# Kernel tuning notes

Measured on AMD Instinct MI355X. Metric: run time of the kernel, lower is better.

The kernel has to match this reference:

```python
import jax, jax.numpy as jnp
import numpy as np

DIM, A, B_FAC, BATCH = 256, 8, 8, 2048
IN_F, OUT_F = A * DIM, B_FAC * DIM  # 2048, 2048


def _make_masks():
    ri = np.arange(IN_F) // A       # input block index per row
    cj = np.arange(OUT_F) // B_FAC  # output block index per col
    diag = ri[:, None] == cj[None, :]
    off = ri[:, None] < cj[None, :]
    return diag, off

DIAG_NP, OFF_NP = _make_masks()
DIAG_M = jnp.asarray(DIAG_NP)
OFF_M = jnp.asarray(OFF_NP)


def setup_inputs() -> dict:
    key = jax.random.key(0)
    k1, k2, k3, k4 = jax.random.split(key, 4)
    x = jax.random.normal(k1, (BATCH, IN_F), dtype=jnp.float32)
    accum_blocks = jax.random.normal(k2, (BATCH, DIM, A, A), dtype=jnp.float32)
    # parameter init mirrors the torch module
    w = jax.random.normal(k3, (IN_F, OUT_F), dtype=jnp.float32) / np.sqrt(IN_F + OUT_F)
    weight = jnp.where(DIAG_M, jnp.log(jnp.abs(w)), w)
    log_diag = jnp.log(jax.random.uniform(k4, (1, OUT_F), dtype=jnp.float32,
                                          minval=0.01, maxval=1.0))
    bias = jnp.zeros((1, OUT_F), dtype=jnp.float32)
    return {"x": x, "accum_blocks": accum_blocks, "weight": weight,
            "log_diag": log_diag, "bias": bias}


def log_dot_exp(lx, ly):
    # result[...,i,j] = logsumexp_k(lx[...,i,k] + ly[...,k,j]); stable via max-shift + GEMM
    mx = jnp.max(lx, axis=-1, keepdims=True)   # [B,D,i,1]
    my = jnp.max(ly, axis=-2, keepdims=True)   # [B,D,1,j]
    s = jnp.einsum('bdik,bdkj->bdij', jnp.exp(lx - mx), jnp.exp(ly - my))
    return jnp.log(s) + mx + my


def reference(x, accum_blocks, weight, log_diag, bias):
    # masked weight construction: exp on the block diagonal, raw off-diagonal, 0 elsewhere
    w = jnp.where(DIAG_M, jnp.exp(weight), jnp.where(OFF_M, weight, 0.0))
    w_norm = jnp.sqrt(jnp.sum(w * w, axis=-1, keepdims=True))  # [IN_F,1], L2 over output dim
    w_eff = jnp.exp(log_diag) * (w / w_norm)
    # log of the diagonal blocks of the effective weight
    ldb_full = log_diag + weight - jnp.log(w_norm)             # [IN_F, OUT_F]
    ldb = ldb_full[DIAG_NP].reshape(1, DIM, A, B_FAC)          # static bool mask -> static gather
    y = x @ w_eff + bias                                       # [B, OUT_F]
    ldb_b = jnp.broadcast_to(ldb, (x.shape[0], DIM, A, B_FAC))
    accum = log_dot_exp(accum_blocks, ldb_b)                   # [B, DIM, A, B_FAC]
    return y, accum
```

## Files before the change

kernel.cpp:

```cpp
#include <hip/hip_runtime.h>
#include <math.h>

#define IN_F 2048
#define OUT_F 2048
#define BATCH 2048

typedef float4 f4;
typedef __attribute__((ext_vector_type(4))) float f32x4;
typedef __attribute__((ext_vector_type(8))) short bf16x8;

__device__ __forceinline__ unsigned short f2bh(float f) {
    unsigned u = __float_as_uint(f);
    u += 0x7FFF + ((u >> 16) & 1);
    return (unsigned short)(u >> 16);
}
__device__ __forceinline__ float bh2f(unsigned short h) {
    return __uint_as_float(((unsigned)h) << 16);
}

__device__ __forceinline__ void gload16(const char* g, char* l) {
    __builtin_amdgcn_global_load_lds(
        (const __attribute__((address_space(1))) unsigned int*)g,
        (__attribute__((address_space(3))) unsigned int*)l, 16, 0, 0);
}


__global__ __launch_bounds__(256) void prep_rows_k(const float* __restrict__ weight,
                                                   const float* __restrict__ log_diag,
                                                   float* __restrict__ invnorm,
                                                   float* __restrict__ ldb) {
    const int i  = blockIdx.x;
    const int ri = i >> 3;
    const int t  = threadIdx.x;
    const f4* wrow = reinterpret_cast<const f4*>(weight + (size_t)i * OUT_F);
    f4 v0 = wrow[t * 2];
    f4 v1 = wrow[t * 2 + 1];
    float raw[8] = {v0.x, v0.y, v0.z, v0.w, v1.x, v1.y, v1.z, v1.w};

    float ss = 0.0f;
    if (t == ri) {
        #pragma unroll
        for (int e = 0; e < 8; ++e) { float m = expf(raw[e]); ss += m * m; }
    } else if (t > ri) {
        #pragma unroll
        for (int e = 0; e < 8; ++e) ss += raw[e] * raw[e];
    }
    #pragma unroll
    for (int o = 32; o > 0; o >>= 1) ss += __shfl_xor(ss, o, 64);
    __shared__ float part[4];
    if ((t & 63) == 0) part[t >> 6] = ss;
    __syncthreads();
    float total = part[0] + part[1] + part[2] + part[3];
    float norm  = sqrtf(total);

    if (t == 0) invnorm[i] = 1.0f / norm;
    if (t == ri) {
        float logn = logf(norm);
        int a = i & 7;
        #pragma unroll
        for (int b = 0; b < 8; ++b)
            ldb[ri * 64 + a * 8 + b] = log_diag[ri * 8 + b] + raw[b] - logn;
    }
}

__global__ __launch_bounds__(256) void prep_ldb_k(const float* __restrict__ ldb,
                                                  const float* __restrict__ log_diag,
                                                  float* __restrict__ myv,
                                                  float* __restrict__ eY,
                                                  float* __restrict__ expld) {
    int t = blockIdx.x * 256 + threadIdx.x;
    expld[t] = expf(log_diag[t]);
    int d = t >> 3, j = t & 7;
    float m = -INFINITY;
    #pragma unroll
    for (int k = 0; k < 8; ++k) m = fmaxf(m, ldb[d * 64 + k * 8 + j]);
    myv[t] = m;
    #pragma unroll
    for (int k = 0; k < 8; ++k) eY[d * 64 + k * 8 + j] = expf(ldb[d * 64 + k * 8 + j] - m);
}

__global__ __launch_bounds__(256) void conv_x_k(const float* __restrict__ x,
                                                char* __restrict__ scratch) {
    const int gid = blockIdx.x * 256 + threadIdx.x;
    const int c  = gid & 3;
    const int r  = (gid >> 2) & 63;
    const int kt = (gid >> 8) & 63;
    const int mt = gid >> 14;
    const int h  = (c ^ (r >> 1)) & 3;
    const int m  = mt * 64 + r;
    const int k  = kt * 32 + h * 8;
    const f4* xp = reinterpret_cast<const f4*>(x + (size_t)m * IN_F + k);
    f4 a = xp[0], b = xp[1];
    float v[8] = {a.x, a.y, a.z, a.w, b.x, b.y, b.z, b.w};
    bf16x8 h8, l8;
    #pragma unroll
    for (int i = 0; i < 8; ++i) {
        unsigned short hb = f2bh(v[i]);
        h8[i] = (short)hb;
        l8[i] = (short)f2bh(v[i] - bh2f(hb));
    }
    *reinterpret_cast<bf16x8*>(scratch + (size_t)gid * 16) = h8;
    *reinterpret_cast<bf16x8*>(scratch + (8u << 20) + (size_t)gid * 16) = l8;
}

__global__ __launch_bounds__(256) void conv_w_k(const float* __restrict__ weight,
                                                const float* __restrict__ invnorm,
                                                const float* __restrict__ expld,
                                                char* __restrict__ scratch) {
    const int blk = blockIdx.x;
    const int ct  = blk >> 6;
    const int kt  = blk & 63;
    if (kt >= 2 * ct + 2) return;

    __shared__ unsigned short sh_hi[32 * 64], sh_lo[32 * 64];
    const int t  = threadIdx.x;
    const int kr = t >> 3;
    const int ns = (t & 7) * 8;
    const int k  = kt * 32 + kr;
    const int n0 = ct * 64 + ns;
    const int rk = k >> 3;

    const f4* wp = reinterpret_cast<const f4*>(weight + (size_t)k * OUT_F + n0);
    f4 a = wp[0], b = wp[1];
    f4 e0 = *reinterpret_cast<const f4*>(expld + n0);
    f4 e1 = *reinterpret_cast<const f4*>(expld + n0 + 4);
    const float inv = invnorm[k];
    float vv[8] = {a.x, a.y, a.z, a.w, b.x, b.y, b.z, b.w};
    float ee[8] = {e0.x, e0.y, e0.z, e0.w, e1.x, e1.y, e1.z, e1.w};
    #pragma unroll
    for (int i = 0; i < 8; ++i) {
        int cj = (n0 + i) >> 3;
        float v = (cj < rk) ? 0.0f : ((cj == rk) ? __expf(vv[i]) : vv[i]);
        v *= inv * ee[i];
        unsigned short hb = f2bh(v);
        sh_hi[kr * 64 + ns + i] = hb;
        sh_lo[kr * 64 + ns + i] = f2bh(v - bh2f(hb));
    }
    __syncthreads();

    const int r = t >> 2, c = t & 3;
    const int h = (c ^ (r >> 1)) & 3;
    bf16x8 oh, ol;
    #pragma unroll
    for (int i = 0; i < 8; ++i) {
        oh[i] = (short)sh_hi[(h * 8 + i) * 64 + r];
        ol[i] = (short)sh_lo[(h * 8 + i) * 64 + r];
    }
    const size_t tb = (size_t)(ct * 64 + kt) * 4096 + (size_t)t * 16;
    *reinterpret_cast<bf16x8*>(scratch + (16u << 20) + tb) = oh;
    *reinterpret_cast<bf16x8*>(scratch + (24u << 20) + tb) = ol;
}

#define LDS_STEP 24576
__global__ __launch_bounds__(256, 2) void gemm_mfma2_k(const char* __restrict__ scratch,
                                                       const float* __restrict__ bias,
                                                       float* __restrict__ y) {
    __shared__ __align__(16) char lds[2 * LDS_STEP];

    const int b  = blockIdx.x;
    const int q  = (b & 7) | (((b >> 8) & 1) << 3);
    const int mt = (b >> 3) & 31;
    const int m0 = mt * 64;
    const int jL = q * 64, jR = (31 - q) * 64;
    const int ctL = q, ctR = 31 - q;
    const int ntL = 2 * (q + 1), nt = 2 * (32 - q);

    const int tid = threadIdx.x;
    const int l   = tid & 63;
    const int w   = tid >> 6;
    const int wr  = w >> 1, wc = w & 1;
    const int l15 = l & 15, h = l >> 4;

    const char* aHi = scratch;
    const char* aLo = scratch + (8u  << 20);
    const char* bHi = scratch + (16u << 20);
    const char* bLo = scratch + (24u << 20);

    int raA[2], raB[2];
    #pragma unroll
    for (int mi = 0; mi < 2; ++mi) {
        int row = wr * 32 + mi * 16 + l15;
        raA[mi] = row * 64 + (((h ^ (row >> 1)) & 3) << 4);
    }
    #pragma unroll
    for (int nj = 0; nj < 2; ++nj) {
        int row = wc * 32 + nj * 16 + l15;
        raB[nj] = row * 64 + (((h ^ (row >> 1)) & 3) << 4);
    }

    f32x4 acc[2][4];
    #pragma unroll
    for (int mi = 0; mi < 2; ++mi)
        #pragma unroll
        for (int cc = 0; cc < 4; ++cc) acc[mi][cc] = (f32x4)0.0f;

    const int lane16 = tid << 4;
    const int wbase  = (tid >> 6) << 10;

    auto STAGE = [&](int buf, int ti) {
        char* lb = lds + buf * LDS_STEP + wbase;
        const size_t at = (size_t)(mt * 64 + ti) * 4096 + lane16;
        gload16(aHi + at, lb);
        gload16(aLo + at, lb + 4096);
        const size_t btR = (size_t)(ctR * 64 + ti) * 4096 + lane16;
        gload16(bHi + btR, lb + 12288);
        gload16(bLo + btR, lb + 20480);
        if (ti < ntL) {
            const size_t btL = (size_t)(ctL * 64 + ti) * 4096 + lane16;
            gload16(bHi + btL, lb + 8192);
            gload16(bLo + btL, lb + 16384);
        }
    };

    STAGE(0, 0);
    __syncthreads();

    int cur = 0;
    for (int ti = 0; ti < nt; ++ti) {
        if (ti + 1 < nt) STAGE(cur ^ 1, ti + 1);
        const char* base = lds + cur * LDS_STEP;
        const bool full = (ti < ntL);
        bf16x8 ah[2], al[2], bh[4], bl[4];
        #pragma unroll
        for (int mi = 0; mi < 2; ++mi) {
            ah[mi] = *reinterpret_cast<const bf16x8*>(base + raA[mi]);
            al[mi] = *reinterpret_cast<const bf16x8*>(base + 4096 + raA[mi]);
        }
        #pragma unroll
        for (int nj = 0; nj < 2; ++nj) {
            bh[2 + nj] = *reinterpret_cast<const bf16x8*>(base + 12288 + raB[nj]);
            bl[2 + nj] = *reinterpret_cast<const bf16x8*>(base + 20480 + raB[nj]);
        }
        if (full) {
            #pragma unroll
            for (int nj = 0; nj < 2; ++nj) {
                bh[nj] = *reinterpret_cast<const bf16x8*>(base + 8192  + raB[nj]);
                bl[nj] = *reinterpret_cast<const bf16x8*>(base + 16384 + raB[nj]);
            }
        }
        #pragma unroll
        for (int mi = 0; mi < 2; ++mi)
            #pragma unroll
            for (int cc = 0; cc < 4; ++cc) {
                if (cc >= 2 || full) {
                    acc[mi][cc] = __builtin_amdgcn_mfma_f32_16x16x32_bf16(ah[mi], bh[cc], acc[mi][cc], 0, 0, 0);
                    acc[mi][cc] = __builtin_amdgcn_mfma_f32_16x16x32_bf16(al[mi], bh[cc], acc[mi][cc], 0, 0, 0);
                    acc[mi][cc] = __builtin_amdgcn_mfma_f32_16x16x32_bf16(ah[mi], bl[cc], acc[mi][cc], 0, 0, 0);
                }
            }
        __syncthreads();
        cur ^= 1;
    }

    #pragma unroll
    for (int mi = 0; mi < 2; ++mi)
        #pragma unroll
        for (int cc = 0; cc < 4; ++cc) {
            int col = ((cc < 2) ? jL : jR) + wc * 32 + ((cc & 1) << 4) + l15;
            float bs = bias[col];
            #pragma unroll
            for (int j = 0; j < 4; ++j) {
                int row = m0 + wr * 32 + mi * 16 + (h << 2) + j;
                y[(size_t)row * OUT_F + col] = ((const float*)&acc[mi][cc])[j] + bs;
            }
        }
}

__global__ __launch_bounds__(256) void accum_k(const float* __restrict__ ab,
                                               const float* __restrict__ eY,
                                               const float* __restrict__ myv,
                                               float* __restrict__ out) {
    __shared__ float lsE[32 * 68];
    __shared__ float lsM[256];

    const int blk = blockIdx.x;
    const int t   = threadIdx.x;
    const int d0  = (blk * 32) & 255;

    #pragma unroll
    for (int hh = 0; hh < 2; ++hh) {
        int idx4 = t + hh * 256;
        int lin  = idx4 * 4;
        int dd = lin >> 6, c = lin & 63;
        f4 v = *reinterpret_cast<const f4*>(eY + d0 * 64 + lin);
        *reinterpret_cast<f4*>(&lsE[dd * 68 + c]) = v;
    }
    lsM[t] = myv[d0 * 8 + t];
    __syncthreads();

    const size_t r = (size_t)blk * 256 + t;
    const f4* lxp = reinterpret_cast<const f4*>(ab + r * 8);
    f4 l0 = lxp[0], l1 = lxp[1];
    float lx[8] = {l0.x, l0.y, l0.z, l0.w, l1.x, l1.y, l1.z, l1.w};

    float mx = lx[0];
    #pragma unroll
    for (int k = 1; k < 8; ++k) mx = fmaxf(mx, lx[k]);
    float el[8];
    #pragma unroll
    for (int k = 0; k < 8; ++k) el[k] = __expf(lx[k] - mx);

    const int dd = t >> 3;
    float s[8] = {0, 0, 0, 0, 0, 0, 0, 0};
    #pragma unroll
    for (int k = 0; k < 8; ++k) {
        float e = el[k];
        f4 r0 = *reinterpret_cast<const f4*>(&lsE[dd * 68 + k * 8]);
        f4 r1 = *reinterpret_cast<const f4*>(&lsE[dd * 68 + k * 8 + 4]);
        s[0] = fmaf(e, r0.x, s[0]); s[1] = fmaf(e, r0.y, s[1]);
        s[2] = fmaf(e, r0.z, s[2]); s[3] = fmaf(e, r0.w, s[3]);
        s[4] = fmaf(e, r1.x, s[4]); s[5] = fmaf(e, r1.y, s[5]);
        s[6] = fmaf(e, r1.z, s[6]); s[7] = fmaf(e, r1.w, s[7]);
    }
    f4 m0v = *reinterpret_cast<const f4*>(&lsM[dd * 8]);
    f4 m1v = *reinterpret_cast<const f4*>(&lsM[dd * 8 + 4]);
    f4 o0, o1;
    o0.x = __logf(s[0]) + mx + m0v.x; o0.y = __logf(s[1]) + mx + m0v.y;
    o0.z = __logf(s[2]) + mx + m0v.z; o0.w = __logf(s[3]) + mx + m0v.w;
    o1.x = __logf(s[4]) + mx + m1v.x; o1.y = __logf(s[5]) + mx + m1v.y;
    o1.z = __logf(s[6]) + mx + m1v.z; o1.w = __logf(s[7]) + mx + m1v.w;
    f4* op = reinterpret_cast<f4*>(out + r * 8);
    op[0] = o0; op[1] = o1;
}

extern "C" void kernel_launch(void* const* d_in, const int* in_sizes, int n_in,
                              void* d_out, int out_size, void* d_ws, size_t ws_size,
                              hipStream_t stream) {
    const float* x        = (const float*)d_in[0];
    const float* ab       = (const float*)d_in[1];
    const float* weight   = (const float*)d_in[2];
    const float* log_diag = (const float*)d_in[3];
    const float* bias     = (const float*)d_in[4];

    float* y     = (float*)d_out;
    float* accum = (float*)d_out + (size_t)BATCH * OUT_F;
    char*  scratch = (char*)accum;

    float* ws      = (float*)d_ws;
    float* invnorm = ws;
    float* ldb     = ws + 2048;
    float* expld   = ws + 18432;
    float* myv     = ws + 20480;
    float* eY      = ws + 22528;

    hipLaunchKernelGGL(prep_rows_k, dim3(2048), dim3(256), 0, stream,
                       weight, log_diag, invnorm, ldb);
    hipLaunchKernelGGL(prep_ldb_k, dim3(8), dim3(256), 0, stream,
                       ldb, log_diag, myv, eY, expld);
    hipLaunchKernelGGL(conv_x_k, dim3(2048), dim3(256), 0, stream, x, scratch);
    hipLaunchKernelGGL(conv_w_k, dim3(2048), dim3(256), 0, stream,
                       weight, invnorm, expld, scratch);
    hipLaunchKernelGGL(gemm_mfma2_k, dim3(512), dim3(256), 0, stream,
                       scratch, bias, y);
    hipLaunchKernelGGL(accum_k, dim3(16384), dim3(256), 0, stream,
                       ab, eY, myv, accum);
}
```

Measured before the change: 316.5 us.

## Merge conversion kernels and co-schedule GEMM with accum blocks in one launch

Merges the x-conversion, weight-conversion and ldb-prep kernels into one launch that dispatches on block index. The GEMM and the log-dot-exp accum work also share one launch, so the small accum blocks can fill CUs while the triangular GEMM tiles finish. The bf16 scratch moves from the accum output buffer into the workspace, which lets accum run alongside the GEMM. This cuts launch count and tail idle time, but the accum blocks now reserve the GEMM's full LDS allocation, which can lower their occupancy.

New measurement: 307.9 us. 1.03x faster.

```diff
diff --git a/kernel.cpp b/kernel.cpp
--- a/kernel.cpp
+++ b/kernel.cpp
@@ -63,264 +63,269 @@
     }
 }
 
-__global__ __launch_bounds__(256) void prep_ldb_k(const float* __restrict__ ldb,
-                                                  const float* __restrict__ log_diag,
-                                                  float* __restrict__ myv,
-                                                  float* __restrict__ eY,
-                                                  float* __restrict__ expld) {
+__global__ __launch_bounds__(256) void fused_prep2_k(const float* __restrict__ x,
+                                                     const float* __restrict__ weight,
+                                                     const float* __restrict__ invnorm,
+                                                     const float* __restrict__ ldb,
+                                                     const float* __restrict__ log_diag,
+                                                     float* __restrict__ myv,
+                                                     float* __restrict__ eY,
+                                                     float* __restrict__ expld,
+                                                     char* __restrict__ scratch) {
+    const int b = blockIdx.x;
+    const int tid = threadIdx.x;
+    if (b < 2048) {
+        const int gid = b * 256 + tid;
+        const int c  = gid & 3;
+        const int r  = (gid >> 2) & 63;
+        const int kt = (gid >> 8) & 63;
+        const int mt = gid >> 14;
+        const int h  = (c ^ (r >> 1)) & 3;
+        const int m  = mt * 64 + r;
+        const int k  = kt * 32 + h * 8;
+        const f4* xp = reinterpret_cast<const f4*>(x + (size_t)m * IN_F + k);
+        f4 a = xp[0], bb = xp[1];
+        float v[8] = {a.x, a.y, a.z, a.w, bb.x, bb.y, bb.z, bb.w};
+        bf16x8 h8, l8;
+        #pragma unroll
+        for (int i = 0; i < 8; ++i) {
+            unsigned short hb = f2bh(v[i]);
+            h8[i] = (short)hb;
+            l8[i] = (short)f2bh(v[i] - bh2f(hb));
+        }
+        *reinterpret_cast<bf16x8*>(scratch + (size_t)gid * 16) = h8;
+        *reinterpret_cast<bf16x8*>(scratch + (8u << 20) + (size_t)gid * 16) = l8;
+    } else if (b < 4096) {
+        const int blk = b - 2048;
+        const int ct  = blk >> 6;
+        const int kt  = blk & 63;
+        if (kt >= 2 * ct + 2) return;
+
+        __shared__ unsigned short sh_hi[32 * 64], sh_lo[32 * 64];
+        const int kr = tid >> 3;
+        const int ns = (tid & 7) * 8;
+        const int k  = kt * 32 + kr;
+        const int n0 = ct * 64 + ns;
+        const int rk = k >> 3;
+
+        const f4* wp = reinterpret_cast<const f4*>(weight + (size_t)k * OUT_F + n0);
+        f4 a = wp[0], bb = wp[1];
+        f4 e0 = *reinterpret_cast<const f4*>(expld + n0);
+        f4 e1 = *reinterpret_cast<const f4*>(expld + n0 + 4);
+        const float inv = invnorm[k];
+        float vv[8] = {a.x, a.y, a.z, a.w, bb.x, bb.y, bb.z, bb.w};
+        float ee[8] = {e0.x, e0.y, e0.z, e0.w, e1.x, e1.y, e1.z, e1.w};
+        #pragma unroll
+        for (int i = 0; i < 8; ++i) {
+            int cj = (n0 + i) >> 3;
+            float v = (cj < rk) ? 0.0f : ((cj == rk) ? __expf(vv[i]) : vv[i]);
+            v *= inv * ee[i];
+            unsigned short hb = f2bh(v);
+            sh_hi[kr * 64 + ns + i] = hb;
+            sh_lo[kr * 64 + ns + i] = f2bh(v - bh2f(hb));
+        }
+        __syncthreads();
+
+        const int r = tid >> 2, c = tid & 3;
+        const int h = (c ^ (r >> 1)) & 3;
+        bf16x8 oh, ol;
+        #pragma unroll
+        for (int i = 0; i < 8; ++i) {
+            oh[i] = (short)sh_hi[(h * 8 + i) * 64 + r];
+            ol[i] = (short)sh_lo[(h * 8 + i) * 64 + r];
+        }
+        const size_t tb = (size_t)(ct * 64 + kt) * 4096 + (size_t)tid * 16;
+        *reinterpret_cast<bf16x8*>(scratch + (16u << 20) + tb) = oh;
+        *reinterpret_cast<bf16x8*>(scratch + (24u << 20) + tb) = ol;
+    } else {
+        int t = (b - 4096) * 256 + tid;
+        int d = t >> 3, j = t & 7;
+        float m = -INFINITY;
+        #pragma unroll
+        for (int k = 0; k < 8; ++k) m = fmaxf(m, ldb[d * 64 + k * 8 + j]);
+        myv[t] = m;
+        #pragma unroll
+        for (int k = 0; k < 8; ++k) eY[d * 64 + k * 8 + j] = __expf(ldb[d * 64 + k * 8 + j] - m);
+    }
+}
+
+__global__ void prep_expld_k(const float* __restrict__ log_diag,
+                             float* __restrict__ expld) {
     int t = blockIdx.x * 256 + threadIdx.x;
     expld[t] = expf(log_diag[t]);
-    int d = t >> 3, j = t & 7;
-    float m = -INFINITY;
-    #pragma unroll
-    for (int k = 0; k < 8; ++k) m = fmaxf(m, ldb[d * 64 + k * 8 + j]);
-    myv[t] = m;
-    #pragma unroll
-    for (int k = 0; k < 8; ++k) eY[d * 64 + k * 8 + j] = expf(ldb[d * 64 + k * 8 + j] - m);
-}
-
-__global__ __launch_bounds__(256) void conv_x_k(const float* __restrict__ x,
-                                                char* __restrict__ scratch) {
-    const int gid = blockIdx.x * 256 + threadIdx.x;
-    const int c  = gid & 3;
-    const int r  = (gid >> 2) & 63;
-    const int kt = (gid >> 8) & 63;
-    const int mt = gid >> 14;
-    const int h  = (c ^ (r >> 1)) & 3;
-    const int m  = mt * 64 + r;
-    const int k  = kt * 32 + h * 8;
-    const f4* xp = reinterpret_cast<const f4*>(x + (size_t)m * IN_F + k);
-    f4 a = xp[0], b = xp[1];
-    float v[8] = {a.x, a.y, a.z, a.w, b.x, b.y, b.z, b.w};
-    bf16x8 h8, l8;
-    #pragma unroll
-    for (int i = 0; i < 8; ++i) {
-        unsigned short hb = f2bh(v[i]);
-        h8[i] = (short)hb;
-        l8[i] = (short)f2bh(v[i] - bh2f(hb));
+}
+
+#define LDS_STEP 24576
+__global__ __launch_bounds__(256, 2) void fused_main_k(const char* __restrict__ scratch,
+                                                       const float* __restrict__ bias,
+                                                       float* __restrict__ y,
+                                                       const float* __restrict__ ab,
+                                                       const float* __restrict__ eY,
+                                                       const float* __restrict__ myv,
+                                                       float* __restrict__ out) {
+    __shared__ __align__(16) char lds[2 * LDS_STEP];
+
+    if (blockIdx.x < 512) {
+        const int b  = blockIdx.x;
+        const int q  = (b & 7) | (((b >> 8) & 1) << 3);
+        const int mt = (b >> 3) & 31;
+        const int m0 = mt * 64;
+        const int jL = q * 64, jR = (31 - q) * 64;
+        const int ctL = q, ctR = 31 - q;
+        const int ntL = 2 * (q + 1), nt = 2 * (32 - q);
+
+        const int tid = threadIdx.x;
+        const int l   = tid & 63;
+        const int w   = tid >> 6;
+        const int wr  = w >> 1, wc = w & 1;
+        const int l15 = l & 15, h = l >> 4;
+
+        const char* aHi = scratch;
+        const char* aLo = scratch + (8u  << 20);
+        const char* bHi = scratch + (16u << 20);
+        const char* bLo = scratch + (24u << 20);
+
+        int raA[2], raB[2];
+        #pragma unroll
+        for (int mi = 0; mi < 2; ++mi) {
+            int row = wr * 32 + mi * 16 + l15;
+            raA[mi] = row * 64 + (((h ^ (row >> 1)) & 3) << 4);
+        }
+        #pragma unroll
+        for (int nj = 0; nj < 2; ++nj) {
+            int row = wc * 32 + nj * 16 + l15;
+            raB[nj] = row * 64 + (((h ^ (row >> 1)) & 3) << 4);
+        }
+
+        f32x4 acc[2][4];
+        #pragma unroll
+        for (int mi = 0; mi < 2; ++mi)
+            #pragma unroll
+            for (int cc = 0; cc < 4; ++cc) acc[mi][cc] = (f32x4)0.0f;
+
+        const int lane16 = tid << 4;
+        const int wbase  = (tid >> 6) << 10;
+
+        auto STAGE = [&](int buf, int ti) {
+            char* lb = lds + buf * LDS_STEP + wbase;
+            const size_t at = (size_t)(mt * 64 + ti) * 4096 + lane16;
+            gload16(aHi + at, lb);
+            gload16(aLo + at, lb + 4096);
+            const size_t btR = (size_t)(ctR * 64 + ti) * 4096 + lane16;
+            gload16(bHi + btR, lb + 12288);
+            gload16(bLo + btR, lb + 20480);
+            if (ti < ntL) {
+                const size_t btL = (size_t)(ctL * 64 + ti) * 4096 + lane16;
+                gload16(bHi + btL, lb + 8192);
+                gload16(bLo + btL, lb + 16384);
+            }
+        };
+
+        STAGE(0, 0);
+        __syncthreads();
+
+        int cur = 0;
+        for (int ti = 0; ti < nt; ++ti) {
+            if (ti + 1 < nt) STAGE(cur ^ 1, ti + 1);
+            const char* base = lds + cur * LDS_STEP;
+            const bool full = (ti < ntL);
+            bf16x8 ah[2], al[2], bh[4], bl[4];
+            #pragma unroll
+            for (int mi = 0; mi < 2; ++mi) {
+                ah[mi] = *reinterpret_cast<const bf16x8*>(base + raA[mi]);
+                al[mi] = *reinterpret_cast<const bf16x8*>(base + 4096 + raA[mi]);
+            }
+            #pragma unroll
+            for (int nj = 0; nj < 2; ++nj) {
+                bh[2 + nj] = *reinterpret_cast<const bf16x8*>(base + 12288 + raB[nj]);
+                bl[2 + nj] = *reinterpret_cast<const bf16x8*>(base + 20480 + raB[nj]);
+            }
+            if (full) {
+                #pragma unroll
+                for (int nj = 0; nj < 2; ++nj) {
+                    bh[nj] = *reinterpret_cast<const bf16x8*>(base + 8192  + raB[nj]);
+                    bl[nj] = *reinterpret_cast<const bf16x8*>(base + 16384 + raB[nj]);
+                }
+            }
+            #pragma unroll
+            for (int mi = 0; mi < 2; ++mi)
+                #pragma unroll
+                for (int cc = 0; cc < 4; ++cc) {
+                    if (cc >= 2 || full) {
+                        acc[mi][cc] = __builtin_amdgcn_mfma_f32_16x16x32_bf16(ah[mi], bh[cc], acc[mi][cc], 0, 0, 0);
+                        acc[mi][cc] = __builtin_amdgcn_mfma_f32_16x16x32_bf16(al[mi], bh[cc], acc[mi][cc], 0, 0, 0);
+                        acc[mi][cc] = __builtin_amdgcn_mfma_f32_16x16x32_bf16(ah[mi], bl[cc], acc[mi][cc], 0, 0, 0);
+                    }
+                }
+            __syncthreads();
+            cur ^= 1;
+        }
+
+        #pragma unroll
+        for (int mi = 0; mi < 2; ++mi)
+            #pragma unroll
+            for (int cc = 0; cc < 4; ++cc) {
+                int col = ((cc < 2) ? jL : jR) + wc * 32 + ((cc & 1) << 4) + l15;
+                float bs = bias[col];
+                #pragma unroll
+                for (int j = 0; j < 4; ++j) {
+                    int row = m0 + wr * 32 + mi * 16 + (h << 2) + j;
+                    y[(size_t)row * OUT_F + col] = ((const float*)&acc[mi][cc])[j] + bs;
+                }
+            }
+    } else {
+        float* lsE = reinterpret_cast<float*>(lds);
+        float* lsM = reinterpret_cast<float*>(lds + 8704);
+
+        const int blk = blockIdx.x - 512;
+        const int t   = threadIdx.x;
+        const int d0  = (blk * 32) & 255;
+
+        #pragma unroll
+        for (int hh = 0; hh < 2; ++hh) {
+            int idx4 = t + hh * 256;
+            int lin  = idx4 * 4;
+            int dd = lin >> 6, c = lin & 63;
+            f4 v = *reinterpret_cast<const f4*>(eY + d0 * 64 + lin);
+            *reinterpret_cast<f4*>(&lsE[dd * 68 + c]) = v;
+        }
+        lsM[t] = myv[d0 * 8 + t];
+        __syncthreads();
+
+        const size_t r = (size_t)blk * 256 + t;
+        const f4* lxp = reinterpret_cast<const f4*>(ab + r * 8);
+        f4 l0 = lxp[0], l1 = lxp[1];
+        float lx[8] = {l0.x, l0.y, l0.z, l0.w, l1.x, l1.y, l1.z, l1.w};
+
+        float mx = lx[0];
+        #pragma unroll
+        for (int k = 1; k < 8; ++k) mx = fmaxf(mx, lx[k]);
+        float el[8];
+        #pragma unroll
+        for (int k = 0; k < 8; ++k) el[k] = __expf(lx[k] - mx);
+
+        const int dd = t >> 3;
+        float s[8] = {0, 0, 0, 0, 0, 0, 0, 0};
+        #pragma unroll
+        for (int k = 0; k < 8; ++k) {
+            float e = el[k];
+            f4 r0 = *reinterpret_cast<const f4*>(&lsE[dd * 68 + k * 8]);
+            f4 r1 = *reinterpret_cast<const f4*>(&lsE[dd * 68 + k * 8 + 4]);
+            s[0] = fmaf(e, r0.x, s[0]); s[1] = fmaf(e, r0.y, s[1]);
+            s[2] = fmaf(e, r0.z, s[2]); s[3] = fmaf(e, r0.w, s[3]);
+            s[4] = fmaf(e, r1.x, s[4]); s[5] = fmaf(e, r1.y, s[5]);
+            s[6] = fmaf(e, r1.z, s[6]); s[7] = fmaf(e, r1.w, s[7]);
+        }
+        f4 m0v = *reinterpret_cast<const f4*>(&lsM[dd * 8]);
+        f4 m1v = *reinterpret_cast<const f4*>(&lsM[dd * 8 + 4]);
+        f4 o0, o1;
+        o0.x = __logf(s[0]) + mx + m0v.x; o0.y = __logf(s[1]) + mx + m0v.y;
+        o0.z = __logf(s[2]) + mx + m0v.z; o0.w = __logf(s[3]) + mx + m0v.w;
+        o1.x = __logf(s[4]) + mx + m1v.x; o1.y = __logf(s[5]) + mx + m1v.y;
+        o1.z = __logf(s[6]) + mx + m1v.z; o1.w = __logf(s[7]) + mx + m1v.w;
+        f4* op = reinterpret_cast<f4*>(out + r * 8);
+        op[0] = o0; op[1] = o1;
     }
-    *reinterpret_cast<bf16x8*>(scratch + (size_t)gid * 16) = h8;
-    *reinterpret_cast<bf16x8*>(scratch + (8u << 20) + (size_t)gid * 16) = l8;
-}
-
-__global__ __launch_bounds__(256) void conv_w_k(const float* __restrict__ weight,
-                                                const float* __restrict__ invnorm,
-                                                const float* __restrict__ expld,
-                                                char* __restrict__ scratch) {
-    const int blk = blockIdx.x;
-    const int ct  = blk >> 6;
-    const int kt  = blk & 63;
-    if (kt >= 2 * ct + 2) return;
-
-    __shared__ unsigned short sh_hi[32 * 64], sh_lo[32 * 64];
-    const int t  = threadIdx.x;
-    const int kr = t >> 3;
-    const int ns = (t & 7) * 8;
-    const int k  = kt * 32 + kr;
-    const int n0 = ct * 64 + ns;
-    const int rk = k >> 3;
-
-    const f4* wp = reinterpret_cast<const f4*>(weight + (size_t)k * OUT_F + n0);
-    f4 a = wp[0], b = wp[1];
-    f4 e0 = *reinterpret_cast<const f4*>(expld + n0);
-    f4 e1 = *reinterpret_cast<const f4*>(expld + n0 + 4);
-    const float inv = invnorm[k];
-    float vv[8] = {a.x, a.y, a.z, a.w, b.x, b.y, b.z, b.w};
-    float ee[8] = {e0.x, e0.y, e0.z, e0.w, e1.x, e1.y, e1.z, e1.w};
-    #pragma unroll
-    for (int i = 0; i < 8; ++i) {
-        int cj = (n0 + i) >> 3;
-        float v = (cj < rk) ? 0.0f : ((cj == rk) ? __expf(vv[i]) : vv[i]);
-        v *= inv * ee[i];
-        unsigned short hb = f2bh(v);
-        sh_hi[kr * 64 + ns + i] = hb;
-        sh_lo[kr * 64 + ns + i] = f2bh(v - bh2f(hb));
-    }
-    __syncthreads();
-
-    const int r = t >> 2, c = t & 3;
-    const int h = (c ^ (r >> 1)) & 3;
-    bf16x8 oh, ol;
-    #pragma unroll
-    for (int i = 0; i < 8; ++i) {
-        oh[i] = (short)sh_hi[(h * 8 + i) * 64 + r];
-        ol[i] = (short)sh_lo[(h * 8 + i) * 64 + r];
-    }
-    const size_t tb = (size_t)(ct * 64 + kt) * 4096 + (size_t)t * 16;
-    *reinterpret_cast<bf16x8*>(scratch + (16u << 20) + tb) = oh;
-    *reinterpret_cast<bf16x8*>(scratch + (24u << 20) + tb) = ol;
-}
-
-#define LDS_STEP 24576
-__global__ __launch_bounds__(256, 2) void gemm_mfma2_k(const char* __restrict__ scratch,
-                                                       const float* __restrict__ bias,
-                                                       float* __restrict__ y) {
-    __shared__ __align__(16) char lds[2 * LDS_STEP];
-
-    const int b  = blockIdx.x;
-    const int q  = (b & 7) | (((b >> 8) & 1) << 3);
-    const int mt = (b >> 3) & 31;
-    const int m0 = mt * 64;
-    const int jL = q * 64, jR = (31 - q) * 64;
-    const int ctL = q, ctR = 31 - q;
-    const int ntL = 2 * (q + 1), nt = 2 * (32 - q);
-
-    const int tid = threadIdx.x;
-    const int l   = tid & 63;
-    const int w   = tid >> 6;
-    const int wr  = w >> 1, wc = w & 1;
-    const int l15 = l & 15, h = l >> 4;
-
-    const char* aHi = scratch;
-    const char* aLo = scratch + (8u  << 20);
-    const char* bHi = scratch + (16u << 20);
-    const char* bLo = scratch + (24u << 20);
-
-    int raA[2], raB[2];
-    #pragma unroll
-    for (int mi = 0; mi < 2; ++mi) {
-        int row = wr * 32 + mi * 16 + l15;
-        raA[mi] = row * 64 + (((h ^ (row >> 1)) & 3) << 4);
-    }
-    #pragma unroll
-    for (int nj = 0; nj < 2; ++nj) {
-        int row = wc * 32 + nj * 16 + l15;
-        raB[nj] = row * 64 + (((h ^ (row >> 1)) & 3) << 4);
-    }
-
-    f32x4 acc[2][4];
-    #pragma unroll
-    for (int mi = 0; mi < 2; ++mi)
-        #pragma unroll
-        for (int cc = 0; cc < 4; ++cc) acc[mi][cc] = (f32x4)0.0f;
-
-    const int lane16 = tid << 4;
-    const int wbase  = (tid >> 6) << 10;
-
-    auto STAGE = [&](int buf, int ti) {
-        char* lb = lds + buf * LDS_STEP + wbase;
-        const size_t at = (size_t)(mt * 64 + ti) * 4096 + lane16;
-        gload16(aHi + at, lb);
-        gload16(aLo + at, lb + 4096);
-        const size_t btR = (size_t)(ctR * 64 + ti) * 4096 + lane16;
-        gload16(bHi + btR, lb + 12288);
-        gload16(bLo + btR, lb + 20480);
-        if (ti < ntL) {
-            const size_t btL = (size_t)(ctL * 64 + ti) * 4096 + lane16;
-            gload16(bHi + btL, lb + 8192);
-            gload16(bLo + btL, lb + 16384);
-        }
-    };
-
-    STAGE(0, 0);
-    __syncthreads();
-
-    int cur = 0;
-    for (int ti = 0; ti < nt; ++ti) {
-        if (ti + 1 < nt) STAGE(cur ^ 1, ti + 1);
-        const char* base = lds + cur * LDS_STEP;
-        const bool full = (ti < ntL);
-        bf16x8 ah[2], al[2], bh[4], bl[4];
-        #pragma unroll
-        for (int mi = 0; mi < 2; ++mi) {
-            ah[mi] = *reinterpret_cast<const bf16x8*>(base + raA[mi]);
-            al[mi] = *reinterpret_cast<const bf16x8*>(base + 4096 + raA[mi]);
-        }
-        #pragma unroll
-        for (int nj = 0; nj < 2; ++nj) {
-            bh[2 + nj] = *reinterpret_cast<const bf16x8*>(base + 12288 + raB[nj]);
-            bl[2 + nj] = *reinterpret_cast<const bf16x8*>(base + 20480 + raB[nj]);
-        }
-        if (full) {
-            #pragma unroll
-            for (int nj = 0; nj < 2; ++nj) {
-                bh[nj] = *reinterpret_cast<const bf16x8*>(base + 8192  + raB[nj]);
-                bl[nj] = *reinterpret_cast<const bf16x8*>(base + 16384 + raB[nj]);
-            }
-        }
-        #pragma unroll
-        for (int mi = 0; mi < 2; ++mi)
-            #pragma unroll
-            for (int cc = 0; cc < 4; ++cc) {
-                if (cc >= 2 || full) {
-                    acc[mi][cc] = __builtin_amdgcn_mfma_f32_16x16x32_bf16(ah[mi], bh[cc], acc[mi][cc], 0, 0, 0);
-                    acc[mi][cc] = __builtin_amdgcn_mfma_f32_16x16x32_bf16(al[mi], bh[cc], acc[mi][cc], 0, 0, 0);
-                    acc[mi][cc] = __builtin_amdgcn_mfma_f32_16x16x32_bf16(ah[mi], bl[cc], acc[mi][cc], 0, 0, 0);
-                }
-            }
-        __syncthreads();
-        cur ^= 1;
-    }
-
-    #pragma unroll
-    for (int mi = 0; mi < 2; ++mi)
-        #pragma unroll
-        for (int cc = 0; cc < 4; ++cc) {
-            int col = ((cc < 2) ? jL : jR) + wc * 32 + ((cc & 1) << 4) + l15;
-            float bs = bias[col];
-            #pragma unroll
-            for (int j = 0; j < 4; ++j) {
-                int row = m0 + wr * 32 + mi * 16 + (h << 2) + j;
-                y[(size_t)row * OUT_F + col] = ((const float*)&acc[mi][cc])[j] + bs;
-            }
-        }
-}
-
-__global__ __launch_bounds__(256) void accum_k(const float* __restrict__ ab,
-                                               const float* __restrict__ eY,
-                                               const float* __restrict__ myv,
-                                               float* __restrict__ out) {
-    __shared__ float lsE[32 * 68];
-    __shared__ float lsM[256];
-
-    const int blk = blockIdx.x;
-    const int t   = threadIdx.x;
-    const int d0  = (blk * 32) & 255;
-
-    #pragma unroll
-    for (int hh = 0; hh < 2; ++hh) {
-        int idx4 = t + hh * 256;
-        int lin  = idx4 * 4;
-        int dd = lin >> 6, c = lin & 63;
-        f4 v = *reinterpret_cast<const f4*>(eY + d0 * 64 + lin);
-        *reinterpret_cast<f4*>(&lsE[dd * 68 + c]) = v;
-    }
-    lsM[t] = myv[d0 * 8 + t];
-    __syncthreads();
-
-    const size_t r = (size_t)blk * 256 + t;
-    const f4* lxp = reinterpret_cast<const f4*>(ab + r * 8);
-    f4 l0 = lxp[0], l1 = lxp[1];
-    float lx[8] = {l0.x, l0.y, l0.z, l0.w, l1.x, l1.y, l1.z, l1.w};
-
-    float mx = lx[0];
-    #pragma unroll
-    for (int k = 1; k < 8; ++k) mx = fmaxf(mx, lx[k]);
-    float el[8];
-    #pragma unroll
-    for (int k = 0; k < 8; ++k) el[k] = __expf(lx[k] - mx);
-
-    const int dd = t >> 3;
-    float s[8] = {0, 0, 0, 0, 0, 0, 0, 0};
-    #pragma unroll
-    for (int k = 0; k < 8; ++k) {
-        float e = el[k];
-        f4 r0 = *reinterpret_cast<const f4*>(&lsE[dd * 68 + k * 8]);
-        f4 r1 = *reinterpret_cast<const f4*>(&lsE[dd * 68 + k * 8 + 4]);
-        s[0] = fmaf(e, r0.x, s[0]); s[1] = fmaf(e, r0.y, s[1]);
-        s[2] = fmaf(e, r0.z, s[2]); s[3] = fmaf(e, r0.w, s[3]);
-        s[4] = fmaf(e, r1.x, s[4]); s[5] = fmaf(e, r1.y, s[5]);
-        s[6] = fmaf(e, r1.z, s[6]); s[7] = fmaf(e, r1.w, s[7]);
-    }
-    f4 m0v = *reinterpret_cast<const f4*>(&lsM[dd * 8]);
-    f4 m1v = *reinterpret_cast<const f4*>(&lsM[dd * 8 + 4]);
-    f4 o0, o1;
-    o0.x = __logf(s[0]) + mx + m0v.x; o0.y = __logf(s[1]) + mx + m0v.y;
-    o0.z = __logf(s[2]) + mx + m0v.z; o0.w = __logf(s[3]) + mx + m0v.w;
-    o1.x = __logf(s[4]) + mx + m1v.x; o1.y = __logf(s[5]) + mx + m1v.y;
-    o1.z = __logf(s[6]) + mx + m1v.z; o1.w = __logf(s[7]) + mx + m1v.w;
-    f4* op = reinterpret_cast<f4*>(out + r * 8);
-    op[0] = o0; op[1] = o1;
 }
 
 extern "C" void kernel_launch(void* const* d_in, const int* in_sizes, int n_in,
@@ -334,7 +339,6 @@
 
     float* y     = (float*)d_out;
     float* accum = (float*)d_out + (size_t)BATCH * OUT_F;
-    char*  scratch = (char*)accum;
 
     float* ws      = (float*)d_ws;
     float* invnorm = ws;
@@ -342,16 +346,14 @@
     float* expld   = ws + 18432;
     float* myv     = ws + 20480;
     float* eY      = ws + 22528;
-
+    char*  scratch = (char*)d_ws + (1u << 20);
+
+    hipLaunchKernelGGL(prep_expld_k, dim3(8), dim3(256), 0, stream,
+                       log_diag, expld);
     hipLaunchKernelGGL(prep_rows_k, dim3(2048), dim3(256), 0, stream,
                        weight, log_diag, invnorm, ldb);
-    hipLaunchKernelGGL(prep_ldb_k, dim3(8), dim3(256), 0, stream,
-                       ldb, log_diag, myv, eY, expld);
-    hipLaunchKernelGGL(conv_x_k, dim3(2048), dim3(256), 0, stream, x, scratch);
-    hipLaunchKernelGGL(conv_w_k, dim3(2048), dim3(256), 0, stream,
-                       weight, invnorm, expld, scratch);
-    hipLaunchKernelGGL(gemm_mfma2_k, dim3(512), dim3(256), 0, stream,
-                       scratch, bias, y);
-    hipLaunchKernelGGL(accum_k, dim3(16384), dim3(256), 0, stream,
-                       ab, eY, myv, accum);
-}
+    hipLaunchKernelGGL(fused_prep2_k, dim3(4104), dim3(256), 0, stream,
+                       x, weight, invnorm, ldb, log_diag, myv, eY, expld, scratch);
+    hipLaunchKernelGGL(fused_main_k, dim3(16896), dim3(256), 0, stream,
+                       scratch, bias, y, ab, eY, myv, accum);
+}
```
